# Kernel optimization log

Hardware: AMD Instinct MI355X
Metric: run time of the kernel (lower is better)

Reference implementation:

```python
import jax, jax.numpy as jnp
import numpy as np

L = 6          # num_layers
B = 2          # batch
F = 16         # num_frames
T = 64         # num_tokens per frame
S = F * T      # seq len = 1024
E = 768        # embed_dim
H = 12         # num_heads
DK = 64        # d_k
DV = 64        # d_v
DFF = 3072     # d_ff
EPS = 1e-5


def setup_inputs() -> dict:
    key = jax.random.key(0)
    ks = jax.random.split(key, 14)
    std = 0.02
    return {
        "x": jax.random.normal(ks[0], (B, S, E), jnp.float32),
        "t_pos": jax.random.normal(ks[1], (1, F, E), jnp.float32) * std,
        "s_pos": jax.random.normal(ks[2], (1, T, E), jnp.float32) * std,
        "Wq": jax.random.normal(ks[3], (L, E, H * DK), jnp.float32) * std,
        "Wk": jax.random.normal(ks[4], (L, E, H * DK), jnp.float32) * std,
        "Wv": jax.random.normal(ks[5], (L, E, H * DV), jnp.float32) * std,
        "Wo": jax.random.normal(ks[6], (L, H * DV, E), jnp.float32) * std,
        "ln1_g": jnp.ones((L, E), jnp.float32),
        "ln1_b": jnp.zeros((L, E), jnp.float32),
        "W1": jax.random.normal(ks[7], (L, E, DFF), jnp.float32) * std,
        "W2": jax.random.normal(ks[8], (L, DFF, E), jnp.float32) * std,
        "ln2_g": jnp.ones((L, E), jnp.float32),
        "ln2_b": jnp.zeros((L, E), jnp.float32),
    }


def _ln(x, g, b):
    m = jnp.mean(x, axis=-1, keepdims=True)
    v = jnp.mean(jnp.square(x - m), axis=-1, keepdims=True)
    return (x - m) * jax.lax.rsqrt(v + EPS) * g + b


def reference(x, t_pos, s_pos, Wq, Wk, Wv, Wo, ln1_g, ln1_b, W1, W2, ln2_g, ln2_b):
    # positional embeddings: frame emb repeated per token, token emb tiled per frame
    t_emb = jnp.repeat(t_pos, T, axis=1)          # [1, S, E]
    s_emb = jnp.tile(s_pos, (1, F, 1))            # [1, S, E]
    x = x + t_emb + s_emb

    # combined causal + pad mask (pad: first embed channel == 0)
    causal = jnp.triu(jnp.ones((S, S), bool), 1)[None, :, :]      # [1, S, S]
    pad = (x[:, :, 0] == 0.0)[:, None, :]                          # [B, 1, S]
    mask = (causal | pad)[:, None, :, :]                           # [B, 1, S, S]

    scale = 1.0 / np.sqrt(DK).astype(np.float32)
    attns = []
    for l in range(L):
        q = (x @ Wq[l]).reshape(B, S, H, DK).transpose(0, 2, 1, 3)  # [B,H,S,DK]
        k = (x @ Wk[l]).reshape(B, S, H, DK).transpose(0, 2, 1, 3)
        v = (x @ Wv[l]).reshape(B, S, H, DV).transpose(0, 2, 1, 3)
        scores = jnp.einsum("bhqd,bhkd->bhqk", q, k) * scale
        scores = jnp.where(mask, -1e9, scores)
        attn = jax.nn.softmax(scores, axis=-1)                      # [B,H,S,S]
        ctx = jnp.einsum("bhqk,bhkd->bhqd", attn, v)
        ctx = ctx.transpose(0, 2, 1, 3).reshape(B, S, H * DV)
        x = _ln(ctx @ Wo[l] + x, ln1_g[l], ln1_b[l])
        h = jax.nn.relu(x @ W1[l]) @ W2[l]
        x = _ln(h + x, ln2_g[l], ln2_b[l])
        attns.append(attn)
    return x, jnp.stack(attns)  # [B,S,E], [L,B,H,S,S]
```

## Files before the change

kernel.cpp:

```cpp
#include <hip/hip_runtime.h>
#include <hip/hip_bf16.h>

#define LYR  6
#define BATCH 2
#define TOK  64
#define SEQ  1024
#define EMB  768
#define HEADS 12
#define HDK  64
#define DFF  3072
#define QKVN 2304

typedef __bf16 bf16_t;
typedef __bf16 bf16x8 __attribute__((ext_vector_type(8)));
typedef float  f32x4  __attribute__((ext_vector_type(4)));
typedef unsigned int u32;

#define GLDS16(g, l) __builtin_amdgcn_global_load_lds( \
    (const __attribute__((address_space(1))) u32*)(g), \
    (__attribute__((address_space(3))) u32*)(l), 16, 0, 0)

static __device__ __forceinline__ unsigned short bfbits(float f) {
    bf16_t b = (bf16_t)f; return *(unsigned short*)&b;
}
static __device__ __forceinline__ float loadf(const void* p, size_t e, int f32) {
    if (f32) return ((const float*)p)[e];
    return (float)((const bf16_t*)p)[e];
}
static __device__ __forceinline__ ushort4 load4bf(const void* p, size_t e, int f32) {
    if (f32) {
        float4 f = *(const float4*)((const float*)p + e);
        ushort4 u; u.x = bfbits(f.x); u.y = bfbits(f.y); u.z = bfbits(f.z); u.w = bfbits(f.w);
        return u;
    }
    return *(const ushort4*)((const unsigned short*)p + e);
}

__global__ __launch_bounds__(256)
void detect_k(const void* w, int* flag)
{
    __shared__ int bad;
    if (threadIdx.x == 0) bad = 0;
    __syncthreads();
    const unsigned short* p = (const unsigned short*)w;
    int local = 0;
    for (int i = threadIdx.x; i < 4096; i += 256) {
        float v = (float)(*(const bf16_t*)&p[i]);
        if (!(v < 1e3f && v > -1e3f)) local = 1;
    }
    if (local) atomicOr(&bad, 1);
    __syncthreads();
    if (threadIdx.x == 0) *flag = bad;
}

__global__ __launch_bounds__(256)
void transp_k(const void* __restrict__ src, bf16_t* __restrict__ dst,
              int K, int N, long sstride, long dstride, long drow0, long dld,
              const int* __restrict__ flagp)
{
    __shared__ unsigned short sm[64][68];
    const int f32 = *flagp;
    const int l  = blockIdx.z;
    const int n0 = blockIdx.x * 64;
    const int k0 = blockIdx.y * 64;
    const int tid = threadIdx.x;
    const int rr = tid >> 4;
    const int cc = tid & 15;

    const size_t sb = (size_t)l * sstride;
#pragma unroll
    for (int p = 0; p < 4; p++) {
        const int kr = rr + p * 16;
        ushort4 u = load4bf(src, sb + (size_t)(k0 + kr) * N + n0 + cc * 4, f32);
        *(ushort4*)&sm[kr][cc * 4] = u;
    }
    __syncthreads();
    const size_t db = (size_t)l * dstride;
#pragma unroll
    for (int p = 0; p < 4; p++) {
        const int r2 = rr + p * 16;
        ushort4 v;
        v.x = sm[cc * 4 + 0][r2];
        v.y = sm[cc * 4 + 1][r2];
        v.z = sm[cc * 4 + 2][r2];
        v.w = sm[cc * 4 + 3][r2];
        *(ushort4*)&dst[db + (size_t)(drow0 + n0 + r2) * dld + k0 + cc * 4] = v;
    }
}

template<int EPI>
__global__ __launch_bounds__(256)
void gemm_k(const bf16_t* __restrict__ A, long lda,
            const bf16_t* __restrict__ BT, long ldb,
            void* __restrict__ C, long ldc, int K)
{
    __shared__ __align__(16) unsigned short As[128 * 32];
    __shared__ __align__(16) unsigned short Bs[64 * 32];

    const int tid  = threadIdx.x;
    const int lane = tid & 63;
    const int wave = tid >> 6;
    const int bm = blockIdx.x * 128;
    const int bn = blockIdx.y * 64;

    const int srow = lane >> 2;
    const int scb  = (lane & 3) * 16;

    const char* gA = (const char*)A;
    const char* gB = (const char*)BT;

    f32x4 acc[2][4];
#pragma unroll
    for (int af = 0; af < 2; af++)
#pragma unroll
        for (int bf = 0; bf < 4; bf++) acc[af][bf] = (f32x4){0.f, 0.f, 0.f, 0.f};

    const int l15 = lane & 15, l4 = lane >> 4;

    for (int k0 = 0; k0 < K; k0 += 32) {
#pragma unroll
        for (int j = 0; j < 2; j++) {
            const int rb = (j * 4 + wave) * 16;
            const char* g = gA + ((size_t)(bm + rb + srow) * lda + k0) * 2 + scb;
            GLDS16(g, &As[rb * 32]);
        }
        {
            const int rb = wave * 16;
            const char* g = gB + ((size_t)(bn + rb + srow) * ldb + k0) * 2 + scb;
            GLDS16(g, &Bs[rb * 32]);
        }
        __syncthreads();

        const bf16x8 a0 = *(const bf16x8*)&As[(wave * 32 + l15) * 32 + l4 * 8];
        const bf16x8 a1 = *(const bf16x8*)&As[(wave * 32 + 16 + l15) * 32 + l4 * 8];
#pragma unroll
        for (int bf = 0; bf < 4; bf++) {
            const bf16x8 bv = *(const bf16x8*)&Bs[(bf * 16 + l15) * 32 + l4 * 8];
            acc[0][bf] = __builtin_amdgcn_mfma_f32_16x16x32_bf16(a0, bv, acc[0][bf], 0, 0, 0);
            acc[1][bf] = __builtin_amdgcn_mfma_f32_16x16x32_bf16(a1, bv, acc[1][bf], 0, 0, 0);
        }
        __syncthreads();
    }

#pragma unroll
    for (int af = 0; af < 2; af++) {
#pragma unroll
        for (int bf = 0; bf < 4; bf++) {
#pragma unroll
            for (int r = 0; r < 4; r++) {
                const int row = bm + wave * 32 + af * 16 + l4 * 4 + r;
                const int col = bn + bf * 16 + l15;
                const float v = acc[af][bf][r];
                const size_t idx = (size_t)row * ldc + col;
                if constexpr (EPI == 0) {
                    ((bf16_t*)C)[idx] = (bf16_t)v;
                } else if constexpr (EPI == 1) {
                    ((bf16_t*)C)[idx] = (bf16_t)(v > 0.f ? v : 0.f);
                } else {
                    ((float*)C)[idx] = v;
                }
            }
        }
    }
}

__global__ __launch_bounds__(256)
void posadd_k(const void* __restrict__ x, const void* __restrict__ tp,
              const void* __restrict__ sp, float* __restrict__ X,
              bf16_t* __restrict__ XB, int* __restrict__ pad,
              const int* __restrict__ flagp)
{
    const int f32 = *flagp;
    const int row = blockIdx.x;
    const int s = row % SEQ;
    const int f = s / TOK, tt = s % TOK;
    const int tid = threadIdx.x;
#pragma unroll
    for (int i = 0; i < 3; i++) {
        int e = tid + i * 256;
        float v = loadf(x, (size_t)row * EMB + e, f32)
                + loadf(tp, (size_t)f * EMB + e, f32)
                + loadf(sp, (size_t)tt * EMB + e, f32);
        X[(size_t)row * EMB + e]  = v;
        XB[(size_t)row * EMB + e] = (bf16_t)v;
        if (e == 0) pad[row] = (v == 0.0f) ? 1 : 0;
    }
}

__global__ __launch_bounds__(256)
void attn_k(const bf16_t* __restrict__ QKV, long ldx, bf16_t* __restrict__ CTX,
            void* __restrict__ outp, long probs_off,
            const int* __restrict__ pad, const int* __restrict__ flagp)
{
    __shared__ __align__(16) unsigned short KV[64][72];
    __shared__ __align__(16) unsigned short P[16][1032];
    __shared__ float redm[4][16];
    __shared__ float reds[4][16];

    const int f32 = *flagp;
    const int bx  = blockIdx.x;
    const int z   = blockIdx.y;
    const int bq  = z / HEADS, h = z % HEADS;
    const int tid = threadIdx.x;
    const int lane = tid & 63;
    const int w    = tid >> 6;
    const int l15  = lane & 15;
    const int l4   = lane >> 4;

    const size_t xoff = (size_t)bq * SEQ * ldx + (size_t)h * HDK;
    const bf16_t* Qp = QKV + xoff;
    const bf16_t* Kp = QKV + xoff + EMB;
    const bf16_t* Vp = QKV + xoff + 2 * EMB;
    const int row0 = bx * 16;
    const int nt   = (bx >> 2) + 1;

    bf16x8 aq0, aq1;
    {
        const bf16_t* qp = Qp + (size_t)(row0 + l15) * ldx + l4 * 8;
        aq0 = *(const bf16x8*)qp;
        aq1 = *(const bf16x8*)(qp + 32);
    }

    f32x4 sc[16];

#pragma unroll
    for (int ct = 0; ct < 16; ct++) {
        if (ct < nt) {
            {
                const int tk = tid >> 3, d0 = (tid & 7) * 8;
                const bf16_t* kp = Kp + (size_t)(ct * 64 + tk) * ldx + d0;
                *(uint4*)&KV[tk][d0]      = *(const uint4*)kp;
                *(uint4*)&KV[tk + 32][d0] = *(const uint4*)(kp + (size_t)32 * ldx);
            }
            __syncthreads();
            bf16x8 b0 = *(const bf16x8*)&KV[w * 16 + l15][l4 * 8];
            bf16x8 b1 = *(const bf16x8*)&KV[w * 16 + l15][32 + l4 * 8];
            f32x4 a = (f32x4){0.f, 0.f, 0.f, 0.f};
            a = __builtin_amdgcn_mfma_f32_16x16x32_bf16(aq0, b0, a, 0, 0, 0);
            a = __builtin_amdgcn_mfma_f32_16x16x32_bf16(aq1, b1, a, 0, 0, 0);
            const int col = ct * 64 + w * 16 + l15;
            const int pd  = pad[bq * SEQ + col];
#pragma unroll
            for (int r = 0; r < 4; r++) {
                float v = a[r] * 0.125f;
                if (col > row0 + l4 * 4 + r || pd) v = -1e9f;
                sc[ct][r] = v;
            }
            __syncthreads();
        }
    }

    float m4[4], s4[4];
#pragma unroll
    for (int r = 0; r < 4; r++) m4[r] = -3.0e38f;
#pragma unroll
    for (int ct = 0; ct < 16; ct++)
        if (ct < nt) {
#pragma unroll
            for (int r = 0; r < 4; r++) m4[r] = fmaxf(m4[r], sc[ct][r]);
        }
#pragma unroll
    for (int r = 0; r < 4; r++) {
        m4[r] = fmaxf(m4[r], __shfl_xor(m4[r], 1, 64));
        m4[r] = fmaxf(m4[r], __shfl_xor(m4[r], 2, 64));
        m4[r] = fmaxf(m4[r], __shfl_xor(m4[r], 4, 64));
        m4[r] = fmaxf(m4[r], __shfl_xor(m4[r], 8, 64));
    }
    if (l15 == 0) {
#pragma unroll
        for (int r = 0; r < 4; r++) redm[w][l4 * 4 + r] = m4[r];
    }
    __syncthreads();
#pragma unroll
    for (int r = 0; r < 4; r++) {
        const int row = l4 * 4 + r;
        m4[r] = fmaxf(fmaxf(redm[0][row], redm[1][row]),
                      fmaxf(redm[2][row], redm[3][row]));
        s4[r] = 0.f;
    }
#pragma unroll
    for (int ct = 0; ct < 16; ct++)
        if (ct < nt) {
#pragma unroll
            for (int r = 0; r < 4; r++) {
                float e = __expf(sc[ct][r] - m4[r]);
                sc[ct][r] = e;
                s4[r] += e;
            }
        }
#pragma unroll
    for (int r = 0; r < 4; r++) {
        s4[r] += __shfl_xor(s4[r], 1, 64);
        s4[r] += __shfl_xor(s4[r], 2, 64);
        s4[r] += __shfl_xor(s4[r], 4, 64);
        s4[r] += __shfl_xor(s4[r], 8, 64);
    }
    if (l15 == 0) {
#pragma unroll
        for (int r = 0; r < 4; r++) reds[w][l4 * 4 + r] = s4[r];
    }
    __syncthreads();
    float inv[4];
#pragma unroll
    for (int r = 0; r < 4; r++) {
        const int row = l4 * 4 + r;
        inv[r] = 1.0f / (reds[0][row] + reds[1][row] + reds[2][row] + reds[3][row]);
    }

    const size_t obase = (size_t)probs_off + ((size_t)z * SEQ + row0) * SEQ;
#pragma unroll
    for (int ct = 0; ct < 16; ct++) {
        if (ct < nt) {
            const int col = ct * 64 + w * 16 + l15;
#pragma unroll
            for (int r = 0; r < 4; r++) {
                const int row = l4 * 4 + r;
                const float p  = sc[ct][r] * inv[r];
                const float p2 = __shfl_xor(p, 1, 64);
                if (!(lane & 1)) {
                    const unsigned int pk =
                        ((unsigned int)bfbits(p2) << 16) | bfbits(p);
                    *(unsigned int*)&P[row][col] = pk;
                    if (!f32)
                        *(unsigned int*)((unsigned short*)outp + obase +
                                         (size_t)row * SEQ + col) = pk;
                }
                if (f32)
                    ((float*)outp)[obase + (size_t)row * SEQ + col] = p;
            }
        }
    }
    {
        const int c0 = nt * 64;
        if (c0 < SEQ) {
            const int rr = tid >> 4, ii = tid & 15;
            if (f32) {
                float* op = (float*)outp + obase + (size_t)rr * SEQ;
                const float4 zz = {0.f, 0.f, 0.f, 0.f};
                for (int c = c0 + ii * 4; c < SEQ; c += 64) *(float4*)(op + c) = zz;
            } else {
                unsigned short* op = (unsigned short*)outp + obase + (size_t)rr * SEQ;
                const uint4 zz = {0u, 0u, 0u, 0u};
                for (int c = c0 + ii * 8; c < SEQ; c += 128) *(uint4*)(op + c) = zz;
            }
        }
    }

    f32x4 co = (f32x4){0.f, 0.f, 0.f, 0.f};
#pragma unroll
    for (int kt = 0; kt < 16; kt++) {
        if (kt < nt) {
            __syncthreads();
#pragma unroll
            for (int i = 0; i < 4; i++) {
                const int e = (tid + i * 256) * 4;
                const int kk = e >> 6, n = e & 63;
                const ushort4 u = *(const ushort4*)
                    ((const unsigned short*)Vp + (size_t)(kt * 64 + kk) * ldx + n);
                KV[n + 0][kk] = u.x; KV[n + 1][kk] = u.y;
                KV[n + 2][kk] = u.z; KV[n + 3][kk] = u.w;
            }
            __syncthreads();
            bf16x8 a0 = *(const bf16x8*)&P[l15][kt * 64 + l4 * 8];
            bf16x8 a1 = *(const bf16x8*)&P[l15][kt * 64 + 32 + l4 * 8];
            bf16x8 b0 = *(const bf16x8*)&KV[w * 16 + l15][l4 * 8];
            bf16x8 b1 = *(const bf16x8*)&KV[w * 16 + l15][32 + l4 * 8];
            co = __builtin_amdgcn_mfma_f32_16x16x32_bf16(a0, b0, co, 0, 0, 0);
            co = __builtin_amdgcn_mfma_f32_16x16x32_bf16(a1, b1, co, 0, 0, 0);
        }
    }
    bf16_t* cp = CTX + (size_t)bq * SEQ * EMB + (size_t)h * HDK
               + (size_t)row0 * EMB + w * 16 + l15;
#pragma unroll
    for (int r = 0; r < 4; r++)
        cp[(size_t)(l4 * 4 + r) * EMB] = (bf16_t)co[r];
}

static __device__ __forceinline__ float bsum(float v, float* red)
{
#pragma unroll
    for (int off = 32; off; off >>= 1) v += __shfl_down(v, off, 64);
    const int lane = threadIdx.x & 63, w = threadIdx.x >> 6;
    __syncthreads();
    if (lane == 0) red[w] = v;
    __syncthreads();
    return red[0] + red[1] + red[2] + red[3];
}

__global__ __launch_bounds__(256)
void ln_k(const float* __restrict__ proj, float* __restrict__ X,
          bf16_t* __restrict__ XB, const void* __restrict__ g, long goff,
          const void* __restrict__ bb, long boff2, const int* __restrict__ flagp)
{
    const int f32 = *flagp;
    const int row = blockIdx.x;
    const float* p = proj + (size_t)row * EMB;
    float* x  = X  + (size_t)row * EMB;
    bf16_t* xb = XB + (size_t)row * EMB;
    const int tid = threadIdx.x;
    __shared__ float red[4];

    float v[3];
    float sum = 0.f;
#pragma unroll
    for (int i = 0; i < 3; i++) { int e = tid + i * 256; v[i] = p[e] + x[e]; sum += v[i]; }
    sum = bsum(sum, red);
    const float mean = sum * (1.0f / EMB);

    float vs = 0.f;
#pragma unroll
    for (int i = 0; i < 3; i++) { float d = v[i] - mean; vs += d * d; }
    vs = bsum(vs, red);
    const float rstd = rsqrtf(vs * (1.0f / EMB) + 1e-5f);

#pragma unroll
    for (int i = 0; i < 3; i++) {
        int e = tid + i * 256;
        float y = (v[i] - mean) * rstd * loadf(g, goff + e, f32) + loadf(bb, boff2 + e, f32);
        x[e] = y;
        xb[e] = (bf16_t)y;
    }
}

__global__ __launch_bounds__(256)
void copyout_k(const float* __restrict__ X, void* __restrict__ outp,
               const int* __restrict__ flagp)
{
    const int f32 = *flagp;
    int i = blockIdx.x * 256 + threadIdx.x;
    float v = X[i];
    if (f32) ((float*)outp)[i] = v;
    else     ((bf16_t*)outp)[i] = (bf16_t)v;
}

extern "C" void kernel_launch(void* const* d_in, const int* in_sizes, int n_in,
                              void* d_out, int out_size, void* d_ws, size_t ws_size,
                              hipStream_t stream)
{
    const void* x  = d_in[0];
    const void* tp = d_in[1];
    const void* sp = d_in[2];
    const void* Wq = d_in[3];
    const void* Wk = d_in[4];
    const void* Wv = d_in[5];
    const void* Wo = d_in[6];
    const void* g1 = d_in[7];
    const void* b1 = d_in[8];
    const void* W1 = d_in[9];
    const void* W2 = d_in[10];
    const void* g2 = d_in[11];
    const void* b2 = d_in[12];

    const size_t BS   = (size_t)BATCH * SEQ;
    const size_t BSE  = BS * EMB;
    const size_t ATT1 = (size_t)BATCH * HEADS * SEQ * SEQ;

    char* ws = (char*)d_ws;
    size_t off = 0;
    auto alloc = [&](size_t bytes) { void* p = ws + off; off += (bytes + 255) & ~255ULL; return p; };

    float*  X     = (float*)alloc(BSE * 4);
    bf16_t* XB    = (bf16_t*)alloc(BSE * 2);
    bf16_t* QKV   = (bf16_t*)alloc(BS * QKVN * 2);
    bf16_t* CTXB  = (bf16_t*)alloc(BSE * 2);
    bf16_t* HB    = (bf16_t*)alloc(BS * DFF * 2);
    float*  PRJ   = (float*)alloc(BSE * 4);
    bf16_t* WqkvT = (bf16_t*)alloc((size_t)LYR * QKVN * EMB * 2);
    bf16_t* WoT   = (bf16_t*)alloc((size_t)LYR * EMB * EMB * 2);
    bf16_t* W1T   = (bf16_t*)alloc((size_t)LYR * DFF * EMB * 2);
    bf16_t* W2T   = (bf16_t*)alloc((size_t)LYR * EMB * DFF * 2);
    int*    pad   = (int*)alloc(BS * 4);
    int*    flag  = (int*)alloc(256);

    detect_k<<<dim3(1), 256, 0, stream>>>(Wq, flag);

    transp_k<<<dim3(12, 12, LYR), 256, 0, stream>>>(
        Wq, WqkvT, EMB, EMB, (long)EMB * EMB, (long)QKVN * EMB, 0, EMB, flag);
    transp_k<<<dim3(12, 12, LYR), 256, 0, stream>>>(
        Wk, WqkvT, EMB, EMB, (long)EMB * EMB, (long)QKVN * EMB, EMB, EMB, flag);
    transp_k<<<dim3(12, 12, LYR), 256, 0, stream>>>(
        Wv, WqkvT, EMB, EMB, (long)EMB * EMB, (long)QKVN * EMB, 2 * EMB, EMB, flag);
    transp_k<<<dim3(12, 12, LYR), 256, 0, stream>>>(
        Wo, WoT, EMB, EMB, (long)EMB * EMB, (long)EMB * EMB, 0, EMB, flag);
    transp_k<<<dim3(DFF / 64, 12, LYR), 256, 0, stream>>>(
        W1, W1T, EMB, DFF, (long)EMB * DFF, (long)DFF * EMB, 0, EMB, flag);
    transp_k<<<dim3(12, DFF / 64, LYR), 256, 0, stream>>>(
        W2, W2T, DFF, EMB, (long)DFF * EMB, (long)EMB * DFF, 0, DFF, flag);

    posadd_k<<<dim3((int)BS), 256, 0, stream>>>(x, tp, sp, X, XB, pad, flag);

    for (int l = 0; l < LYR; l++) {
        const long probs_off = (long)(BSE + (size_t)l * ATT1);

        gemm_k<0><<<dim3(16, QKVN / 64), 256, 0, stream>>>(
            XB, EMB, WqkvT + (size_t)l * QKVN * EMB, EMB, QKV, QKVN, EMB);

        attn_k<<<dim3(SEQ / 16, BATCH * HEADS), 256, 0, stream>>>(
            QKV, QKVN, CTXB, d_out, probs_off, pad, flag);

        gemm_k<2><<<dim3(16, EMB / 64), 256, 0, stream>>>(
            CTXB, EMB, WoT + (size_t)l * EMB * EMB, EMB, PRJ, EMB, EMB);
        ln_k<<<dim3((int)BS), 256, 0, stream>>>(PRJ, X, XB, g1, (long)l * EMB, b1, (long)l * EMB, flag);

        gemm_k<1><<<dim3(16, DFF / 64), 256, 0, stream>>>(
            XB, EMB, W1T + (size_t)l * DFF * EMB, EMB, HB, DFF, EMB);
        gemm_k<2><<<dim3(16, EMB / 64), 256, 0, stream>>>(
            HB, DFF, W2T + (size_t)l * EMB * DFF, DFF, PRJ, EMB, DFF);
        ln_k<<<dim3((int)BS), 256, 0, stream>>>(PRJ, X, XB, g2, (long)l * EMB, b2, (long)l * EMB, flag);
    }

    copyout_k<<<dim3((int)(BSE / 256)), 256, 0, stream>>>(X, d_out, flag);
}
```

Baseline: 2.006 ms.

## Add 128x128 GEMM tile for wide GEMMs and pre-transpose V for attention

Adds a 128x128-tile GEMM variant, with four waves in a 2x2 arrangement each computing a 64x64 sub-tile. It is used for the QKV and W1 projections to raise per-block data reuse, at the cost of fewer blocks (288 and 384) on the GPU. A new kernel transposes V per head into a [z][d][seq] buffer once per layer. Attention then reads K and V^T fragments directly from global memory instead of staging them through shared memory, which removes most per-tile barriers and the scattered V transpose writes. The trade is an extra launch and buffer round-trip, and more uncoalesced global reads inside attention.

```diff
diff --git a/kernel.cpp b/kernel.cpp
--- a/kernel.cpp
+++ b/kernel.cpp
@@ -88,11 +88,42 @@
     }
 }
 
+__global__ __launch_bounds__(256)
+void vtr_k(const bf16_t* __restrict__ QKV, bf16_t* __restrict__ VT)
+{
+    __shared__ unsigned short sm[64][68];
+    const int z  = blockIdx.y;
+    const int s0 = blockIdx.x * 64;
+    const int bq = z / HEADS, h = z % HEADS;
+    const int tid = threadIdx.x;
+    const int rr = tid >> 4, cc = tid & 15;
+    const unsigned short* src = (const unsigned short*)QKV
+        + (size_t)bq * SEQ * QKVN + 2 * EMB + (size_t)h * HDK;
+#pragma unroll
+    for (int p = 0; p < 4; p++) {
+        const int s = rr + p * 16;
+        *(ushort4*)&sm[s][cc * 4] =
+            *(const ushort4*)(src + (size_t)(s0 + s) * QKVN + cc * 4);
+    }
+    __syncthreads();
+    unsigned short* dst = (unsigned short*)VT + (size_t)z * HDK * SEQ;
+#pragma unroll
+    for (int p = 0; p < 4; p++) {
+        const int d = rr + p * 16;
+        ushort4 v;
+        v.x = sm[cc * 4 + 0][d];
+        v.y = sm[cc * 4 + 1][d];
+        v.z = sm[cc * 4 + 2][d];
+        v.w = sm[cc * 4 + 3][d];
+        *(ushort4*)(dst + (size_t)d * SEQ + s0 + cc * 4) = v;
+    }
+}
+
 template<int EPI>
 __global__ __launch_bounds__(256)
-void gemm_k(const bf16_t* __restrict__ A, long lda,
-            const bf16_t* __restrict__ BT, long ldb,
-            void* __restrict__ C, long ldc, int K)
+void gemm64_k(const bf16_t* __restrict__ A, long lda,
+              const bf16_t* __restrict__ BT, long ldb,
+              void* __restrict__ C, long ldc, int K)
 {
     __shared__ __align__(16) unsigned short As[128 * 32];
     __shared__ __align__(16) unsigned short Bs[64 * 32];
@@ -102,9 +133,9 @@
     const int wave = tid >> 6;
     const int bm = blockIdx.x * 128;
     const int bn = blockIdx.y * 64;
-
     const int srow = lane >> 2;
     const int scb  = (lane & 3) * 16;
+    const int l15 = lane & 15, l4 = lane >> 4;
 
     const char* gA = (const char*)A;
     const char* gB = (const char*)BT;
@@ -114,8 +145,6 @@
     for (int af = 0; af < 2; af++)
 #pragma unroll
         for (int bf = 0; bf < 4; bf++) acc[af][bf] = (f32x4){0.f, 0.f, 0.f, 0.f};
-
-    const int l15 = lane & 15, l4 = lane >> 4;
 
     for (int k0 = 0; k0 < K; k0 += 32) {
 #pragma unroll
@@ -164,6 +193,86 @@
     }
 }
 
+template<int EPI>
+__global__ __launch_bounds__(256)
+void gemm128_k(const bf16_t* __restrict__ A, long lda,
+               const bf16_t* __restrict__ BT, long ldb,
+               void* __restrict__ C, long ldc, int K)
+{
+    __shared__ __align__(16) unsigned short As[128 * 32];
+    __shared__ __align__(16) unsigned short Bs[128 * 32];
+
+    const int tid  = threadIdx.x;
+    const int lane = tid & 63;
+    const int wave = tid >> 6;
+    const int bm = blockIdx.x * 128;
+    const int bn = blockIdx.y * 128;
+    const int srow = lane >> 2;
+    const int scb  = (lane & 3) * 16;
+    const int l15 = lane & 15, l4 = lane >> 4;
+    const int wr = wave >> 1, wc = wave & 1;
+
+    const char* gA = (const char*)A;
+    const char* gB = (const char*)BT;
+
+    f32x4 acc[4][4];
+#pragma unroll
+    for (int m = 0; m < 4; m++)
+#pragma unroll
+        for (int n = 0; n < 4; n++) acc[m][n] = (f32x4){0.f, 0.f, 0.f, 0.f};
+
+    for (int k0 = 0; k0 < K; k0 += 32) {
+#pragma unroll
+        for (int j = 0; j < 2; j++) {
+            const int rb = (j * 4 + wave) * 16;
+            const char* g = gA + ((size_t)(bm + rb + srow) * lda + k0) * 2 + scb;
+            GLDS16(g, &As[rb * 32]);
+        }
+#pragma unroll
+        for (int j = 0; j < 2; j++) {
+            const int rb = (j * 4 + wave) * 16;
+            const char* g = gB + ((size_t)(bn + rb + srow) * ldb + k0) * 2 + scb;
+            GLDS16(g, &Bs[rb * 32]);
+        }
+        __syncthreads();
+
+        bf16x8 a[4], b[4];
+#pragma unroll
+        for (int m = 0; m < 4; m++)
+            a[m] = *(const bf16x8*)&As[(wr * 64 + m * 16 + l15) * 32 + l4 * 8];
+#pragma unroll
+        for (int n = 0; n < 4; n++)
+            b[n] = *(const bf16x8*)&Bs[(wc * 64 + n * 16 + l15) * 32 + l4 * 8];
+#pragma unroll
+        for (int m = 0; m < 4; m++)
+#pragma unroll
+            for (int n = 0; n < 4; n++)
+                acc[m][n] = __builtin_amdgcn_mfma_f32_16x16x32_bf16(a[m], b[n], acc[m][n], 0, 0, 0);
+        __syncthreads();
+    }
+
+#pragma unroll
+    for (int m = 0; m < 4; m++) {
+#pragma unroll
+        for (int n = 0; n < 4; n++) {
+#pragma unroll
+            for (int r = 0; r < 4; r++) {
+                const int row = bm + wr * 64 + m * 16 + l4 * 4 + r;
+                const int col = bn + wc * 64 + n * 16 + l15;
+                const float v = acc[m][n][r];
+                const size_t idx = (size_t)row * ldc + col;
+                if constexpr (EPI == 0) {
+                    ((bf16_t*)C)[idx] = (bf16_t)v;
+                } else if constexpr (EPI == 1) {
+                    ((bf16_t*)C)[idx] = (bf16_t)(v > 0.f ? v : 0.f);
+                } else {
+                    ((float*)C)[idx] = v;
+                }
+            }
+        }
+    }
+}
+
 __global__ __launch_bounds__(256)
 void posadd_k(const void* __restrict__ x, const void* __restrict__ tp,
               const void* __restrict__ sp, float* __restrict__ X,
@@ -188,11 +297,10 @@
 }
 
 __global__ __launch_bounds__(256)
-void attn_k(const bf16_t* __restrict__ QKV, long ldx, bf16_t* __restrict__ CTX,
-            void* __restrict__ outp, long probs_off,
+void attn_k(const bf16_t* __restrict__ QKV, const bf16_t* __restrict__ VT,
+            bf16_t* __restrict__ CTX, void* __restrict__ outp, long probs_off,
             const int* __restrict__ pad, const int* __restrict__ flagp)
 {
-    __shared__ __align__(16) unsigned short KV[64][72];
     __shared__ __align__(16) unsigned short P[16][1032];
     __shared__ float redm[4][16];
     __shared__ float reds[4][16];
@@ -207,16 +315,16 @@
     const int l15  = lane & 15;
     const int l4   = lane >> 4;
 
-    const size_t xoff = (size_t)bq * SEQ * ldx + (size_t)h * HDK;
-    const bf16_t* Qp = QKV + xoff;
-    const bf16_t* Kp = QKV + xoff + EMB;
-    const bf16_t* Vp = QKV + xoff + 2 * EMB;
+    const size_t qoff = (size_t)bq * SEQ * QKVN + (size_t)h * HDK;
+    const bf16_t* Qp = QKV + qoff;
+    const bf16_t* Kp = QKV + qoff + EMB;
+    const bf16_t* Vt = VT + (size_t)z * HDK * SEQ;
     const int row0 = bx * 16;
     const int nt   = (bx >> 2) + 1;
 
     bf16x8 aq0, aq1;
     {
-        const bf16_t* qp = Qp + (size_t)(row0 + l15) * ldx + l4 * 8;
+        const bf16_t* qp = Qp + (size_t)(row0 + l15) * QKVN + l4 * 8;
         aq0 = *(const bf16x8*)qp;
         aq1 = *(const bf16x8*)(qp + 32);
     }
@@ -226,15 +334,9 @@
 #pragma unroll
     for (int ct = 0; ct < 16; ct++) {
         if (ct < nt) {
-            {
-                const int tk = tid >> 3, d0 = (tid & 7) * 8;
-                const bf16_t* kp = Kp + (size_t)(ct * 64 + tk) * ldx + d0;
-                *(uint4*)&KV[tk][d0]      = *(const uint4*)kp;
-                *(uint4*)&KV[tk + 32][d0] = *(const uint4*)(kp + (size_t)32 * ldx);
-            }
-            __syncthreads();
-            bf16x8 b0 = *(const bf16x8*)&KV[w * 16 + l15][l4 * 8];
-            bf16x8 b1 = *(const bf16x8*)&KV[w * 16 + l15][32 + l4 * 8];
+            const bf16_t* kp = Kp + (size_t)(ct * 64 + w * 16 + l15) * QKVN + l4 * 8;
+            const bf16x8 b0 = *(const bf16x8*)kp;
+            const bf16x8 b1 = *(const bf16x8*)(kp + 32);
             f32x4 a = (f32x4){0.f, 0.f, 0.f, 0.f};
             a = __builtin_amdgcn_mfma_f32_16x16x32_bf16(aq0, b0, a, 0, 0, 0);
             a = __builtin_amdgcn_mfma_f32_16x16x32_bf16(aq1, b1, a, 0, 0, 0);
@@ -246,7 +348,6 @@
                 if (col > row0 + l4 * 4 + r || pd) v = -1e9f;
                 sc[ct][r] = v;
             }
-            __syncthreads();
         }
     }
 
@@ -345,26 +446,17 @@
             }
         }
     }
+    __syncthreads();
 
     f32x4 co = (f32x4){0.f, 0.f, 0.f, 0.f};
 #pragma unroll
     for (int kt = 0; kt < 16; kt++) {
         if (kt < nt) {
-            __syncthreads();
-#pragma unroll
-            for (int i = 0; i < 4; i++) {
-                const int e = (tid + i * 256) * 4;
-                const int kk = e >> 6, n = e & 63;
-                const ushort4 u = *(const ushort4*)
-                    ((const unsigned short*)Vp + (size_t)(kt * 64 + kk) * ldx + n);
-                KV[n + 0][kk] = u.x; KV[n + 1][kk] = u.y;
-                KV[n + 2][kk] = u.z; KV[n + 3][kk] = u.w;
-            }
-            __syncthreads();
-            bf16x8 a0 = *(const bf16x8*)&P[l15][kt * 64 + l4 * 8];
-            bf16x8 a1 = *(const bf16x8*)&P[l15][kt * 64 + 32 + l4 * 8];
-            bf16x8 b0 = *(const bf16x8*)&KV[w * 16 + l15][l4 * 8];
-            bf16x8 b1 = *(const bf16x8*)&KV[w * 16 + l15][32 + l4 * 8];
+            const bf16x8 a0 = *(const bf16x8*)&P[l15][kt * 64 + l4 * 8];
+            const bf16x8 a1 = *(const bf16x8*)&P[l15][kt * 64 + 32 + l4 * 8];
+            const bf16_t* vp = Vt + (size_t)(w * 16 + l15) * SEQ + kt * 64 + l4 * 8;
+            const bf16x8 b0 = *(const bf16x8*)vp;
+            const bf16x8 b1 = *(const bf16x8*)(vp + 32);
             co = __builtin_amdgcn_mfma_f32_16x16x32_bf16(a0, b0, co, 0, 0, 0);
             co = __builtin_amdgcn_mfma_f32_16x16x32_bf16(a1, b1, co, 0, 0, 0);
         }
@@ -462,6 +554,7 @@
     float*  X     = (float*)alloc(BSE * 4);
     bf16_t* XB    = (bf16_t*)alloc(BSE * 2);
     bf16_t* QKV   = (bf16_t*)alloc(BS * QKVN * 2);
+    bf16_t* VT    = (bf16_t*)alloc((size_t)BATCH * HEADS * HDK * SEQ * 2);
     bf16_t* CTXB  = (bf16_t*)alloc(BSE * 2);
     bf16_t* HB    = (bf16_t*)alloc(BS * DFF * 2);
     float*  PRJ   = (float*)alloc(BSE * 4);
@@ -492,19 +585,21 @@
     for (int l = 0; l < LYR; l++) {
         const long probs_off = (long)(BSE + (size_t)l * ATT1);
 
-        gemm_k<0><<<dim3(16, QKVN / 64), 256, 0, stream>>>(
+        gemm128_k<0><<<dim3(16, QKVN / 128), 256, 0, stream>>>(
             XB, EMB, WqkvT + (size_t)l * QKVN * EMB, EMB, QKV, QKVN, EMB);
 
+        vtr_k<<<dim3(SEQ / 64, BATCH * HEADS), 256, 0, stream>>>(QKV, VT);
+
         attn_k<<<dim3(SEQ / 16, BATCH * HEADS), 256, 0, stream>>>(
-            QKV, QKVN, CTXB, d_out, probs_off, pad, flag);
-
-        gemm_k<2><<<dim3(16, EMB / 64), 256, 0, stream>>>(
+            QKV, VT, CTXB, d_out, probs_off, pad, flag);
+
+        gemm64_k<2><<<dim3(16, EMB / 64), 256, 0, stream>>>(
             CTXB, EMB, WoT + (size_t)l * EMB * EMB, EMB, PRJ, EMB, EMB);
         ln_k<<<dim3((int)BS), 256, 0, stream>>>(PRJ, X, XB, g1, (long)l * EMB, b1, (long)l * EMB, flag);
 
-        gemm_k<1><<<dim3(16, DFF / 64), 256, 0, stream>>>(
+        gemm128_k<1><<<dim3(16, DFF / 128), 256, 0, stream>>>(
             XB, EMB, W1T + (size_t)l * DFF * EMB, EMB, HB, DFF, EMB);
-        gemm_k<2><<<dim3(16, EMB / 64), 256, 0, stream>>>(
+        gemm64_k<2><<<dim3(16, EMB / 64), 256, 0, stream>>>(
             HB, DFF, W2T + (size_t)l * EMB * DFF, DFF, PRJ, EMB, DFF);
         ln_k<<<dim3((int)BS), 256, 0, stream>>>(PRJ, X, XB, g2, (long)l * EMB, b2, (long)l * EMB, flag);
     }
```

New measurement: 1.910 ms. 4.8% less time.
